# Performance work log

Hardware: AMD Instinct MI355X
Metric: run time of the kernel (lower is better)

The kernel has to match this reference:

```python
import jax, jax.numpy as jnp
import numpy as np
import math

B, SQ, SK, D_MODEL, OUT_DIM = 8, 2048, 2048, 1024, 128
MASK_VALUE = -1e6  # torch code fills masked scores with -1000000.0, not -inf


def setup_inputs() -> dict:
    key = jax.random.key(0)
    ks = jax.random.split(key, 10)
    scale = 1.0 / math.sqrt(D_MODEL)
    return {
        "queries": jax.random.normal(ks[0], (B, SQ, D_MODEL), dtype=jnp.float32),
        "keys": jax.random.normal(ks[1], (B, SK, D_MODEL), dtype=jnp.float32),
        "values": jax.random.normal(ks[2], (B, SK, D_MODEL), dtype=jnp.float32),
        "valid_lens": jax.random.randint(ks[3], (B,), 1, SK + 1, dtype=jnp.int32),
        "w_q": jax.random.normal(ks[4], (D_MODEL, OUT_DIM), dtype=jnp.float32) * scale,
        "b_q": jnp.zeros((OUT_DIM,), dtype=jnp.float32),
        "w_k": jax.random.normal(ks[5], (D_MODEL, OUT_DIM), dtype=jnp.float32) * scale,
        "b_k": jnp.zeros((OUT_DIM,), dtype=jnp.float32),
        "w_v": jax.random.normal(ks[6], (D_MODEL, OUT_DIM), dtype=jnp.float32) * scale,
        "b_v": jnp.zeros((OUT_DIM,), dtype=jnp.float32),
    }


def reference(queries, keys, values, valid_lens, w_q, b_q, w_k, b_k, w_v, b_v):
    # QKV projections (LazyLinear equivalents)
    Q = queries @ w_q + b_q   # [B, SQ, OUT_DIM]
    K = keys @ w_k + b_k      # [B, SK, OUT_DIM]
    V = values @ w_v + b_v    # [B, SK, OUT_DIM]
    dim = Q.shape[-1]
    scores = jnp.einsum("bqd,bkd->bqk", Q, K) / jnp.sqrt(jnp.asarray(dim, Q.dtype))
    # masked_softmax: valid_lens [B] -> mask positions >= valid_len on the key axis
    mask = jnp.arange(scores.shape[-1])[None, None, :] < valid_lens[:, None, None]
    scores = jnp.where(mask, scores, jnp.asarray(MASK_VALUE, scores.dtype))
    attn = jax.nn.softmax(scores, axis=-1)
    return jnp.einsum("bqk,bkd->bqd", attn, V)  # [B, SQ, OUT_DIM]
```

## Files before the change

### kernel.cpp

```cpp
#include <hip/hip_runtime.h>
#include <math.h>

constexpr int BATCH  = 8;
constexpr int SEQQ   = 2048;
constexpr int SEQK   = 2048;
constexpr int DMODEL = 1024;
constexpr int ODIM   = 128;

typedef __attribute__((ext_vector_type(8))) short bf16x8;
typedef __attribute__((ext_vector_type(4))) float f32x4;

__device__ inline unsigned short f2bf(float f) {
    union { float f; unsigned int u; } v; v.f = f;
    unsigned int r = v.u + 0x7FFFu + ((v.u >> 16) & 1u);
    return (unsigned short)(r >> 16);
}

__device__ __forceinline__ unsigned int pk2bf(float a, float b) {
    unsigned int ua = __float_as_uint(a) + 0x8000u;
    unsigned int ub = __float_as_uint(b) + 0x8000u;
    return __builtin_amdgcn_perm(ub, ua, 0x07060302u);
}

__device__ __forceinline__ void gl_lds16(const void* g, void* l) {
    __builtin_amdgcn_global_load_lds(
        (const __attribute__((address_space(1))) unsigned int*)g,
        (__attribute__((address_space(3))) unsigned int*)l, 16, 0, 0);
}

__global__ __launch_bounds__(256)
void wtrans_kernel(const float* __restrict__ Wq, const float* __restrict__ Wk,
                   const float* __restrict__ Wv, unsigned short* __restrict__ Wt)
{
    const int which = blockIdx.z;
    const float* __restrict__ W = which == 0 ? Wq : (which == 1 ? Wk : Wv);
    unsigned short* __restrict__ dst = Wt + (size_t)which * DMODEL * ODIM;
    const int k0 = blockIdx.x * 32, n0 = blockIdx.y * 32;
    __shared__ unsigned short T[32][36];
    const int t = threadIdx.x;
    const int r = t >> 3, c = (t & 7) * 4;
    float4 w = *(const float4*)(W + (size_t)(k0 + r) * ODIM + n0 + c);
    T[r][c + 0] = f2bf(w.x); T[r][c + 1] = f2bf(w.y);
    T[r][c + 2] = f2bf(w.z); T[r][c + 3] = f2bf(w.w);
    __syncthreads();
    const int n = t >> 3, k4 = (t & 7) * 4;
    ushort4 o;
    o.x = T[k4 + 0][n]; o.y = T[k4 + 1][n];
    o.z = T[k4 + 2][n]; o.w = T[k4 + 3][n];
    *(ushort4*)(dst + (size_t)(n0 + n) * DMODEL + k0 + k4) = o;
}

__global__ __launch_bounds__(256, 2)
void proj_kernel(const float* __restrict__ Aq, const float* __restrict__ Ak,
                 const float* __restrict__ Av,
                 const unsigned short* __restrict__ Wt_all,
                 const float* __restrict__ bq, const float* __restrict__ bk,
                 const float* __restrict__ bv,
                 unsigned short* __restrict__ Qb, unsigned short* __restrict__ Kb,
                 unsigned short* __restrict__ Vt)
{
    const int which = blockIdx.y;
    const float* __restrict__ A    = which == 0 ? Aq : (which == 1 ? Ak : Av);
    const float* __restrict__ bias = which == 0 ? bq : (which == 1 ? bk : bv);
    const unsigned short* __restrict__ Wt = Wt_all + (size_t)which * DMODEL * ODIM;

    const int row0 = blockIdx.x * 32;
    const int t = threadIdx.x, wave = t >> 6, lane = t & 63;
    const int lrow = lane & 15, quad = lane >> 4;
    const int wch = wave * 32;

    __shared__ __align__(16) unsigned short As[32 * 1024];
    __shared__ __align__(16) unsigned short Ws[128 * 64];

    f32x4 acc[2][2];
#pragma unroll
    for (int mt = 0; mt < 2; ++mt)
#pragma unroll
        for (int nt = 0; nt < 2; ++nt)
#pragma unroll
            for (int i = 0; i < 4; ++i) acc[mt][nt][i] = 0.f;

    const unsigned short* wgp[4]; int wloff[4];
#pragma unroll
    for (int j = 0; j < 4; ++j) {
        const int s = j * 256 + t;
        const int wr = s >> 3, wcc = (s & 7) ^ (wr & 7);
        wgp[j]   = Wt + (size_t)wr * DMODEL + wcc * 8;
        wloff[j] = s * 8;
    }

#pragma unroll
    for (int j = 0; j < 4; ++j) gl_lds16(wgp[j], &Ws[wloff[j]]);

    {
        const float* abase = A + (size_t)row0 * DMODEL + t * 4;
        const int cb = t >> 1, h = t & 1;
#pragma unroll 1
        for (int bb = 0; bb < 4; ++bb) {
            float4 v[8];
#pragma unroll
            for (int u = 0; u < 8; ++u)
                v[u] = *(const float4*)(abase + (size_t)(bb * 8 + u) * DMODEL);
#pragma unroll
            for (int u = 0; u < 8; ++u) {
                const int j = bb * 8 + u;
                uint2 p;
                p.x = pk2bf(v[u].x, v[u].y);
                p.y = pk2bf(v[u].z, v[u].w);
                *(uint2*)&As[j * 1024 + ((cb ^ (j & 7)) << 3) + h * 4] = p;
            }
        }
    }
    __syncthreads();

    const int x3 = lrow & 7;
    const int rA0 = lrow, rA1 = 16 + lrow;
    const int sw0 = rA0 & 7, sw1 = rA1 & 7;

    for (int s = 0; s < 16; ++s) {
#pragma unroll
        for (int ks = 0; ks < 2; ++ks) {
            const int cf = s * 8 + ks * 4 + quad;
            bf16x8 af0 = *(const bf16x8*)&As[rA0 * 1024 + ((cf ^ sw0) << 3)];
            bf16x8 af1 = *(const bf16x8*)&As[rA1 * 1024 + ((cf ^ sw1) << 3)];
#pragma unroll
            for (int nt = 0; nt < 2; ++nt) {
                const int n = wch + nt * 16 + lrow;
                bf16x8 wf = *(const bf16x8*)&Ws[(n * 8 + ((ks * 4 + quad) ^ x3)) * 8];
                acc[0][nt] = __builtin_amdgcn_mfma_f32_16x16x32_bf16(af0, wf, acc[0][nt], 0, 0, 0);
                acc[1][nt] = __builtin_amdgcn_mfma_f32_16x16x32_bf16(af1, wf, acc[1][nt], 0, 0, 0);
            }
        }
        if (s < 15) {
            asm volatile("s_waitcnt lgkmcnt(0)" ::: "memory");
            __builtin_amdgcn_sched_barrier(0);
            __builtin_amdgcn_s_barrier();
            __builtin_amdgcn_sched_barrier(0);
#pragma unroll
            for (int j = 0; j < 4; ++j)
                gl_lds16(wgp[j] + (s + 1) * 64, &Ws[wloff[j]]);
            asm volatile("s_waitcnt vmcnt(0)" ::: "memory");
            __builtin_amdgcn_sched_barrier(0);
            __builtin_amdgcn_s_barrier();
            __builtin_amdgcn_sched_barrier(0);
        }
    }

    const float sc = (which == 0) ? 0.08838834764831845f : 1.0f;
    float bv_[2];
#pragma unroll
    for (int nt = 0; nt < 2; ++nt) bv_[nt] = bias[wch + nt * 16 + lrow];

    const int b  = row0 >> 11;
    const int mb = row0 & 2047;

    if (which == 2) {
#pragma unroll
        for (int mt = 0; mt < 2; ++mt)
#pragma unroll
            for (int nt = 0; nt < 2; ++nt) {
                const int n = wch + nt * 16 + lrow;
                ushort4 o;
                o.x = f2bf(acc[mt][nt][0] + bv_[nt]);
                o.y = f2bf(acc[mt][nt][1] + bv_[nt]);
                o.z = f2bf(acc[mt][nt][2] + bv_[nt]);
                o.w = f2bf(acc[mt][nt][3] + bv_[nt]);
                *(ushort4*)(Vt + ((size_t)b * ODIM + n) * SEQK
                            + mb + mt * 16 + quad * 4) = o;
            }
    } else {
        unsigned short* __restrict__ Ob = (which == 0) ? Qb : Kb;
#pragma unroll
        for (int mt = 0; mt < 2; ++mt)
#pragma unroll
            for (int nt = 0; nt < 2; ++nt)
#pragma unroll
                for (int r = 0; r < 4; ++r) {
                    float val = sc * (acc[mt][nt][r] + bv_[nt]);
                    Ob[(size_t)(row0 + mt * 16 + quad * 4 + r) * ODIM
                       + wch + nt * 16 + lrow] = f2bf(val);
                }
    }
}

__global__ __launch_bounds__(256, 3)
void flash_kernel(const unsigned short* __restrict__ Qb,
                  const unsigned short* __restrict__ Kb,
                  const unsigned short* __restrict__ Vt,
                  const int* __restrict__ valid_lens,
                  float* __restrict__ Op, float* __restrict__ Lp, int nsplit)
{
    const int b = blockIdx.y, s = blockIdx.z, q0 = blockIdx.x * 64;
    const int skh = SEQK / nsplit;
    const int t = threadIdx.x, wave = t >> 6, lane = t & 63;
    const int lrow = lane & 15, quad = lane >> 4;

    const int valid = valid_lens[b];
    const int vloc  = min(valid - s * skh, skh);

    float* __restrict__ lpart = Lp + (size_t)(s * BATCH + b) * SEQQ + q0;
    float* __restrict__ opart = Op + ((size_t)(s * BATCH + b) * SEQQ + q0) * ODIM;

    if (vloc <= 0) {
        if (t < 64) lpart[t] = 0.f;
        return;
    }

    __shared__ __align__(16) unsigned short Ks[64 * 128];
    __shared__ __align__(16) unsigned short Vs[128 * 64];
    __shared__ __align__(16) unsigned short Ps[4][16][72];

    bf16x8 qf[4];
    {
        const unsigned short* qp =
            Qb + ((size_t)b * SEQQ + q0 + wave * 16 + lrow) * ODIM + quad * 8;
#pragma unroll
        for (int ks = 0; ks < 4; ++ks) qf[ks] = *(const bf16x8*)(qp + ks * 32);
    }

    f32x4 o[8];
#pragma unroll
    for (int nt = 0; nt < 8; ++nt)
#pragma unroll
        for (int i = 0; i < 4; ++i) o[nt][i] = 0.f;
    float lsum[4] = {0.f, 0.f, 0.f, 0.f};

    const unsigned short* kgp[4]; unsigned short* kldst[4];
    const unsigned short* vgp[4]; unsigned short* vldst[4];
    const unsigned short* kbase = Kb + ((size_t)b * SEQK + s * skh) * ODIM;
    const unsigned short* vbase = Vt + (size_t)b * ODIM * SEQK + s * skh;
#pragma unroll
    for (int j = 0; j < 4; ++j) {
        const int sl = j * 256 + t;
        const int kr = sl >> 4, kc = (sl & 15) ^ (kr & 15);
        kgp[j]   = kbase + (size_t)kr * ODIM + kc * 8;
        kldst[j] = &Ks[sl * 8];
        const int vr = sl >> 3, vc = (sl & 7) ^ (vr & 7);
        vgp[j]   = vbase + (size_t)vr * SEQK + vc * 8;
        vldst[j] = &Vs[sl * 8];
    }

    const int x4 = lrow, x3 = lrow & 7;
    const int nch = (vloc + 63) >> 6;

    for (int c = 0; c < nch; ++c) {
        const int k0 = c * 64;
#pragma unroll
        for (int j = 0; j < 4; ++j) {
            gl_lds16(kgp[j] + (size_t)k0 * ODIM, kldst[j]);
            gl_lds16(vgp[j] + k0, vldst[j]);
        }
        __syncthreads();

        f32x4 sv[4];
#pragma unroll
        for (int nt = 0; nt < 4; ++nt)
#pragma unroll
            for (int i = 0; i < 4; ++i) sv[nt][i] = 0.f;
#pragma unroll
        for (int ks = 0; ks < 4; ++ks)
#pragma unroll
            for (int nt = 0; nt < 4; ++nt) {
                const int kr = nt * 16 + lrow;
                const int cc = (ks * 4 + quad) ^ x4;
                bf16x8 kf = *(const bf16x8*)&Ks[(kr * 16 + cc) * 8];
                sv[nt] = __builtin_amdgcn_mfma_f32_16x16x32_bf16(qf[ks], kf, sv[nt], 0, 0, 0);
            }

        if (k0 + 64 > vloc) {
#pragma unroll
            for (int nt = 0; nt < 4; ++nt)
                if (k0 + nt * 16 + lrow >= vloc) {
#pragma unroll
                    for (int i = 0; i < 4; ++i) sv[nt][i] = -1e30f;
                }
        }

#pragma unroll
        for (int nt = 0; nt < 4; ++nt)
#pragma unroll
            for (int r = 0; r < 4; ++r) {
                float p = __expf(sv[nt][r]);
                lsum[r] += p;
                Ps[wave][quad * 4 + r][nt * 16 + lrow] =
                    (unsigned short)((__float_as_uint(p) + 0x8000u) >> 16);
            }

        bf16x8 pf0 = *(const bf16x8*)&Ps[wave][lrow][quad * 8];
        bf16x8 pf1 = *(const bf16x8*)&Ps[wave][lrow][32 + quad * 8];

#pragma unroll
        for (int nt = 0; nt < 8; ++nt) {
            const int vrow = nt * 16 + lrow;
            bf16x8 v0 = *(const bf16x8*)&Vs[(vrow * 8 + (quad ^ x3)) * 8];
            o[nt] = __builtin_amdgcn_mfma_f32_16x16x32_bf16(pf0, v0, o[nt], 0, 0, 0);
        }
#pragma unroll
        for (int nt = 0; nt < 8; ++nt) {
            const int vrow = nt * 16 + lrow;
            bf16x8 v1 = *(const bf16x8*)&Vs[(vrow * 8 + ((4 + quad) ^ x3)) * 8];
            o[nt] = __builtin_amdgcn_mfma_f32_16x16x32_bf16(pf1, v1, o[nt], 0, 0, 0);
        }
        __syncthreads();
    }

#pragma unroll
    for (int msk = 1; msk < 16; msk <<= 1)
#pragma unroll
        for (int r = 0; r < 4; ++r) lsum[r] += __shfl_xor(lsum[r], msk);
    if (lrow == 0) {
#pragma unroll
        for (int r = 0; r < 4; ++r)
            lpart[wave * 16 + quad * 4 + r] = lsum[r];
    }

#pragma unroll
    for (int nt = 0; nt < 8; ++nt)
#pragma unroll
        for (int r = 0; r < 4; ++r)
            opart[(size_t)(wave * 16 + quad * 4 + r) * ODIM + nt * 16 + lrow]
                = o[nt][r];
}

__global__ __launch_bounds__(256)
void combine_kernel(const float* __restrict__ Op, const float* __restrict__ Lp,
                    float* __restrict__ out, int nsplit)
{
    const int idx = blockIdx.x * 256 + threadIdx.x;
    const int row = idx >> 5;
    const size_t SL = (size_t)BATCH * SEQQ;
    float l = 0.f;
    float4 acc = {0.f, 0.f, 0.f, 0.f};
    for (int s = 0; s < nsplit; ++s) {
        float ls = Lp[(size_t)s * SL + row];
        if (ls > 0.f) {
            float4 v = ((const float4*)(Op + (size_t)s * SL * ODIM))[idx];
            acc.x += v.x; acc.y += v.y; acc.z += v.z; acc.w += v.w;
            l += ls;
        }
    }
    const float inv = 1.f / l;
    float4 r;
    r.x = acc.x * inv; r.y = acc.y * inv; r.z = acc.z * inv; r.w = acc.w * inv;
    ((float4*)out)[idx] = r;
}

extern "C" void kernel_launch(void* const* d_in, const int* in_sizes, int n_in,
                              void* d_out, int out_size, void* d_ws, size_t ws_size,
                              hipStream_t stream)
{
    const float* queries    = (const float*)d_in[0];
    const float* keys       = (const float*)d_in[1];
    const float* values     = (const float*)d_in[2];
    const int*   valid_lens = (const int*)d_in[3];
    const float* w_q        = (const float*)d_in[4];
    const float* b_q        = (const float*)d_in[5];
    const float* w_k        = (const float*)d_in[6];
    const float* b_k        = (const float*)d_in[7];
    const float* w_v        = (const float*)d_in[8];
    const float* b_v        = (const float*)d_in[9];
    float* out = (float*)d_out;

    const size_t nQKV = (size_t)BATCH * SEQQ * ODIM;
    unsigned short* Qb = (unsigned short*)d_ws;
    unsigned short* Kb = Qb + nQKV;
    unsigned short* Vt = Kb + nQKV;
    unsigned short* Wt = Vt + nQKV;
    const size_t base = 3 * nQKV * sizeof(unsigned short)
                      + (size_t)3 * DMODEL * ODIM * sizeof(unsigned short);

    int KS = 4;
    if (ws_size < base + 4 * (nQKV * 4 + (size_t)BATCH * SEQQ * 4)) KS = 2;

    float* Op = (float*)((char*)d_ws + base);
    float* Lp = Op + (size_t)KS * nQKV;

    wtrans_kernel<<<dim3(DMODEL / 32, ODIM / 32, 3), 256, 0, stream>>>(w_q, w_k, w_v, Wt);

    proj_kernel<<<dim3((BATCH * SEQQ) / 32, 3), 256, 0, stream>>>(
        queries, keys, values, Wt, b_q, b_k, b_v, Qb, Kb, Vt);

    flash_kernel<<<dim3(SEQQ / 64, BATCH, KS), 256, 0, stream>>>(
        Qb, Kb, Vt, valid_lens, Op, Lp, KS);

    combine_kernel<<<(BATCH * SEQQ * ODIM / 4) / 256, 256, 0, stream>>>(Op, Lp, out, KS);
}
```

Baseline: 268.1 us.

## Rewrite projection GEMM to load operands directly into registers with software prefetch

The projection kernel drops its LDS staging of activations and weights. Each wave now computes 32 rows by all 128 output columns, reading fp32 activations and bf16 weights straight from global memory into registers. Loads are prefetched with register rotation (A two steps ahead, W one step ahead), and each block covers 128 rows instead of 32. This removes LDS traffic and barriers, but gives fewer blocks, heavier register use, and weight reloads per wave that rely on cache hits.

```diff
diff --git a/kernel.cpp b/kernel.cpp
--- a/kernel.cpp
+++ b/kernel.cpp
@@ -1,5 +1,6 @@
 #include <hip/hip_runtime.h>
 #include <math.h>
+
 
 constexpr int BATCH  = 8;
 constexpr int SEQQ   = 2048;
@@ -50,6 +51,38 @@
     *(ushort4*)(dst + (size_t)(n0 + n) * DMODEL + k0 + k4) = o;
 }
 
+#define PST(CA, PA, CW, PW, T, PFA, PFW)                                      \
+  {                                                                            \
+    if (PFA) {                                                                 \
+      const int ko = ((T) + 2) * 32;                                           \
+      _Pragma("unroll")                                                        \
+      for (int mt = 0; mt < 2; ++mt) {                                         \
+        PA[mt][0] = *(const float4*)(ap[mt] + ko);                             \
+        PA[mt][1] = *(const float4*)(ap[mt] + ko + 4);                         \
+      }                                                                        \
+    }                                                                          \
+    if (PFW) {                                                                 \
+      const int kw = ((T) + 1) * 32;                                           \
+      _Pragma("unroll")                                                        \
+      for (int nt = 0; nt < 8; ++nt)                                           \
+        PW[nt] = *(const bf16x8*)(wp + nt * 16 * DMODEL + kw);                 \
+    }                                                                          \
+    bf16x8 af[2];                                                              \
+    _Pragma("unroll")                                                          \
+    for (int mt = 0; mt < 2; ++mt) {                                           \
+      ((unsigned int*)&af[mt])[0] = pk2bf(CA[mt][0].x, CA[mt][0].y);           \
+      ((unsigned int*)&af[mt])[1] = pk2bf(CA[mt][0].z, CA[mt][0].w);           \
+      ((unsigned int*)&af[mt])[2] = pk2bf(CA[mt][1].x, CA[mt][1].y);           \
+      ((unsigned int*)&af[mt])[3] = pk2bf(CA[mt][1].z, CA[mt][1].w);           \
+    }                                                                          \
+    _Pragma("unroll")                                                          \
+    for (int nt = 0; nt < 8; ++nt)                                             \
+      _Pragma("unroll")                                                        \
+      for (int mt = 0; mt < 2; ++mt)                                           \
+        acc[mt][nt] = __builtin_amdgcn_mfma_f32_16x16x32_bf16(                 \
+            af[mt], CW[nt], acc[mt][nt], 0, 0, 0);                             \
+  }
+
 __global__ __launch_bounds__(256, 2)
 void proj_kernel(const float* __restrict__ Aq, const float* __restrict__ Ak,
                  const float* __restrict__ Av,
@@ -64,92 +97,53 @@
     const float* __restrict__ bias = which == 0 ? bq : (which == 1 ? bk : bv);
     const unsigned short* __restrict__ Wt = Wt_all + (size_t)which * DMODEL * ODIM;
 
-    const int row0 = blockIdx.x * 32;
+    const int row0 = blockIdx.x * 128;
     const int t = threadIdx.x, wave = t >> 6, lane = t & 63;
     const int lrow = lane & 15, quad = lane >> 4;
-    const int wch = wave * 32;
-
-    __shared__ __align__(16) unsigned short As[32 * 1024];
-    __shared__ __align__(16) unsigned short Ws[128 * 64];
-
-    f32x4 acc[2][2];
+    const int wrh = wave * 32;
+
+    const float* ap[2];
+    ap[0] = A + (size_t)(row0 + wrh + lrow) * DMODEL + quad * 8;
+    ap[1] = ap[0] + (size_t)16 * DMODEL;
+    const unsigned short* wp = Wt + (size_t)lrow * DMODEL + quad * 8;
+
+    f32x4 acc[2][8];
 #pragma unroll
     for (int mt = 0; mt < 2; ++mt)
 #pragma unroll
-        for (int nt = 0; nt < 2; ++nt)
+        for (int nt = 0; nt < 8; ++nt)
 #pragma unroll
             for (int i = 0; i < 4; ++i) acc[mt][nt][i] = 0.f;
 
-    const unsigned short* wgp[4]; int wloff[4];
-#pragma unroll
-    for (int j = 0; j < 4; ++j) {
-        const int s = j * 256 + t;
-        const int wr = s >> 3, wcc = (s & 7) ^ (wr & 7);
-        wgp[j]   = Wt + (size_t)wr * DMODEL + wcc * 8;
-        wloff[j] = s * 8;
-    }
-
-#pragma unroll
-    for (int j = 0; j < 4; ++j) gl_lds16(wgp[j], &Ws[wloff[j]]);
-
-    {
-        const float* abase = A + (size_t)row0 * DMODEL + t * 4;
-        const int cb = t >> 1, h = t & 1;
-#pragma unroll 1
-        for (int bb = 0; bb < 4; ++bb) {
-            float4 v[8];
-#pragma unroll
-            for (int u = 0; u < 8; ++u)
-                v[u] = *(const float4*)(abase + (size_t)(bb * 8 + u) * DMODEL);
-#pragma unroll
-            for (int u = 0; u < 8; ++u) {
-                const int j = bb * 8 + u;
-                uint2 p;
-                p.x = pk2bf(v[u].x, v[u].y);
-                p.y = pk2bf(v[u].z, v[u].w);
-                *(uint2*)&As[j * 1024 + ((cb ^ (j & 7)) << 3) + h * 4] = p;
-            }
-        }
-    }
-    __syncthreads();
-
-    const int x3 = lrow & 7;
-    const int rA0 = lrow, rA1 = 16 + lrow;
-    const int sw0 = rA0 & 7, sw1 = rA1 & 7;
-
-    for (int s = 0; s < 16; ++s) {
-#pragma unroll
-        for (int ks = 0; ks < 2; ++ks) {
-            const int cf = s * 8 + ks * 4 + quad;
-            bf16x8 af0 = *(const bf16x8*)&As[rA0 * 1024 + ((cf ^ sw0) << 3)];
-            bf16x8 af1 = *(const bf16x8*)&As[rA1 * 1024 + ((cf ^ sw1) << 3)];
-#pragma unroll
-            for (int nt = 0; nt < 2; ++nt) {
-                const int n = wch + nt * 16 + lrow;
-                bf16x8 wf = *(const bf16x8*)&Ws[(n * 8 + ((ks * 4 + quad) ^ x3)) * 8];
-                acc[0][nt] = __builtin_amdgcn_mfma_f32_16x16x32_bf16(af0, wf, acc[0][nt], 0, 0, 0);
-                acc[1][nt] = __builtin_amdgcn_mfma_f32_16x16x32_bf16(af1, wf, acc[1][nt], 0, 0, 0);
-            }
-        }
-        if (s < 15) {
-            asm volatile("s_waitcnt lgkmcnt(0)" ::: "memory");
-            __builtin_amdgcn_sched_barrier(0);
-            __builtin_amdgcn_s_barrier();
-            __builtin_amdgcn_sched_barrier(0);
-#pragma unroll
-            for (int j = 0; j < 4; ++j)
-                gl_lds16(wgp[j] + (s + 1) * 64, &Ws[wloff[j]]);
-            asm volatile("s_waitcnt vmcnt(0)" ::: "memory");
-            __builtin_amdgcn_sched_barrier(0);
-            __builtin_amdgcn_s_barrier();
-            __builtin_amdgcn_sched_barrier(0);
-        }
-    }
+    float4 Aa[2][2], Ab[2][2], Ac[2][2];
+    bf16x8 Wu[8], Wv_[8];
+
+#pragma unroll
+    for (int mt = 0; mt < 2; ++mt) {
+        Aa[mt][0] = *(const float4*)(ap[mt]);
+        Aa[mt][1] = *(const float4*)(ap[mt] + 4);
+        Ab[mt][0] = *(const float4*)(ap[mt] + 32);
+        Ab[mt][1] = *(const float4*)(ap[mt] + 36);
+    }
+#pragma unroll
+    for (int nt = 0; nt < 8; ++nt)
+        Wu[nt] = *(const bf16x8*)(wp + nt * 16 * DMODEL);
+
+    for (int kt = 0; kt < 30; kt += 6) {
+        PST(Aa, Ac, Wu, Wv_, kt + 0, 1, 1);
+        PST(Ab, Aa, Wv_, Wu, kt + 1, 1, 1);
+        PST(Ac, Ab, Wu, Wv_, kt + 2, 1, 1);
+        PST(Aa, Ac, Wv_, Wu, kt + 3, 1, 1);
+        PST(Ab, Aa, Wu, Wv_, kt + 4, 1, 1);
+        PST(Ac, Ab, Wv_, Wu, kt + 5, 1, 1);
+    }
+    PST(Aa, Ac, Wu, Wv_, 30, 0, 1);
+    PST(Ab, Aa, Wv_, Wu, 31, 0, 0);
 
     const float sc = (which == 0) ? 0.08838834764831845f : 1.0f;
-    float bv_[2];
-#pragma unroll
-    for (int nt = 0; nt < 2; ++nt) bv_[nt] = bias[wch + nt * 16 + lrow];
+    float bv_[8];
+#pragma unroll
+    for (int nt = 0; nt < 8; ++nt) bv_[nt] = bias[nt * 16 + lrow];
 
     const int b  = row0 >> 11;
     const int mb = row0 & 2047;
@@ -158,27 +152,27 @@
 #pragma unroll
         for (int mt = 0; mt < 2; ++mt)
 #pragma unroll
-            for (int nt = 0; nt < 2; ++nt) {
-                const int n = wch + nt * 16 + lrow;
+            for (int nt = 0; nt < 8; ++nt) {
+                const int n = nt * 16 + lrow;
                 ushort4 o;
                 o.x = f2bf(acc[mt][nt][0] + bv_[nt]);
                 o.y = f2bf(acc[mt][nt][1] + bv_[nt]);
                 o.z = f2bf(acc[mt][nt][2] + bv_[nt]);
                 o.w = f2bf(acc[mt][nt][3] + bv_[nt]);
                 *(ushort4*)(Vt + ((size_t)b * ODIM + n) * SEQK
-                            + mb + mt * 16 + quad * 4) = o;
+                            + mb + wrh + mt * 16 + quad * 4) = o;
             }
     } else {
         unsigned short* __restrict__ Ob = (which == 0) ? Qb : Kb;
 #pragma unroll
         for (int mt = 0; mt < 2; ++mt)
 #pragma unroll
-            for (int nt = 0; nt < 2; ++nt)
+            for (int nt = 0; nt < 8; ++nt)
 #pragma unroll
                 for (int r = 0; r < 4; ++r) {
                     float val = sc * (acc[mt][nt][r] + bv_[nt]);
-                    Ob[(size_t)(row0 + mt * 16 + quad * 4 + r) * ODIM
-                       + wch + nt * 16 + lrow] = f2bf(val);
+                    Ob[(size_t)(row0 + wrh + mt * 16 + quad * 4 + r) * ODIM
+                       + nt * 16 + lrow] = f2bf(val);
                 }
     }
 }
@@ -377,7 +371,7 @@
 
     wtrans_kernel<<<dim3(DMODEL / 32, ODIM / 32, 3), 256, 0, stream>>>(w_q, w_k, w_v, Wt);
 
-    proj_kernel<<<dim3((BATCH * SEQQ) / 32, 3), 256, 0, stream>>>(
+    proj_kernel<<<dim3((BATCH * SEQQ) / 128, 3), 256, 0, stream>>>(
         queries, keys, values, Wt, b_q, b_k, b_v, Qb, Kb, Vt);
 
     flash_kernel<<<dim3(SEQQ / 64, BATCH, KS), 256, 0, stream>>>(
```

Measured after the change: 299.8 us. +11.8%, slower.
